# Kernel optimization log

Hardware: AMD Instinct MI355X
Metric: run time of the kernel (lower is better)

The kernel has to match this reference:

```python
import jax, jax.numpy as jnp
import numpy as np

D_MODEL = 1024
NHEAD = 16
DHEAD = D_MODEL // NHEAD
DFF = 4096
B, S = 2, 2048
R = 25                # local_attention_radius = 5*5
K = 5                 # rel_pos_max_distance
W = 2 * R + 1         # window width
EPS = 1e-5


def setup_inputs() -> dict:
    key = jax.random.key(0)
    ks = jax.random.split(key, 12)
    s = 0.02
    g = lambda k, shape: jax.random.normal(k, shape, jnp.float32) * s
    return {
        "src": jax.random.normal(ks[0], (B, S, D_MODEL), jnp.float32),
        # attention in/out projections (W stored [out,in], applied x @ W.T + b)
        "wq": g(ks[1], (D_MODEL, D_MODEL)), "bq": jnp.zeros((D_MODEL,), jnp.float32),
        "wk": g(ks[2], (D_MODEL, D_MODEL)), "bk": jnp.zeros((D_MODEL,), jnp.float32),
        "wv": g(ks[3], (D_MODEL, D_MODEL)), "bv": jnp.zeros((D_MODEL,), jnp.float32),
        "wo": g(ks[4], (D_MODEL, D_MODEL)), "bo": jnp.zeros((D_MODEL,), jnp.float32),
        # relative position embeddings, ids clipped to [-K, K] -> 2K+1 rows
        "rel_emb": g(ks[5], (2 * K + 1, DHEAD)),
        # FFN
        "w1": g(ks[6], (DFF, D_MODEL)), "b1": jnp.zeros((DFF,), jnp.float32),
        "w2": g(ks[7], (D_MODEL, DFF)), "b2": jnp.zeros((D_MODEL,), jnp.float32),
        # layernorms
        "g1": jnp.ones((D_MODEL,), jnp.float32), "beta1": jnp.zeros((D_MODEL,), jnp.float32),
        "g2": jnp.ones((D_MODEL,), jnp.float32), "beta2": jnp.zeros((D_MODEL,), jnp.float32),
    }


def _layernorm(x, g, b):
    m = x.mean(-1, keepdims=True)
    v = ((x - m) ** 2).mean(-1, keepdims=True)
    return (x - m) * jax.lax.rsqrt(v + EPS) * g + b


def _rel_window_attention(x, wq, bq, wk, bk, wv, bv, wo, bo, rel_emb):
    b, s, d = x.shape

    def proj(w, bias):
        return (x @ w.T + bias).reshape(b, s, NHEAD, DHEAD).transpose(0, 2, 1, 3)

    q = proj(wq, bq)  # [B,H,S,Dh]
    k = proj(wk, bk)
    v = proj(wv, bv)

    offsets = jnp.arange(-R, R + 1)                     # [W]
    j = jnp.arange(s)[:, None] + offsets[None, :]       # [S,W] absolute key index
    valid = (j >= 0) & (j < s)
    jc = jnp.clip(j, 0, s - 1)

    scale = 1.0 / np.sqrt(DHEAD).astype(np.float32)
    k_win = k[:, :, jc]                                 # [B,H,S,W,Dh] banded gather
    scores = jnp.einsum('bhsd,bhswd->bhsw', q, k_win) * scale
    rel_ids = jnp.clip(offsets, -K, K) + K              # [W]
    scores = scores + jnp.einsum('bhsd,wd->bhsw', q, rel_emb[rel_ids]) * scale
    scores = jnp.where(valid[None, None], scores, jnp.float32(-1e30))
    attn = jax.nn.softmax(scores, axis=-1)              # [B,H,S,W]

    v_win = v[:, :, jc]                                 # [B,H,S,W,Dh]
    out = jnp.einsum('bhsw,bhswd->bhsd', attn, v_win)
    out = out.transpose(0, 2, 1, 3).reshape(b, s, d)
    return out @ wo.T + bo


def reference(src, wq, bq, wk, bk, wv, bv, wo, bo, rel_emb,
              w1, b1, w2, b2, g1, beta1, g2, beta2):
    # post-norm (norm_first=False default) transformer block, dropout=0 (eval)
    z = _rel_window_attention(src, wq, bq, wk, bk, wv, bv, wo, bo, rel_emb)
    x = _layernorm(src + z, g1, beta1)
    ff = jax.nn.relu(x @ w1.T + b1) @ w2.T + b2
    return _layernorm(x + ff, g2, beta2)
```

## Files before the change

kernel.cpp:

```cpp
#include <hip/hip_runtime.h>


#define D_MODEL 1024
#define SEQ     2048
#define NROWS   4096
#define WIN     51
#define RAD     25

typedef __attribute__((ext_vector_type(8))) __bf16 bf16x8;
typedef __attribute__((ext_vector_type(4))) float  floatx4;

__device__ __forceinline__ unsigned short f2bf(float x) {
    unsigned u = __float_as_uint(x);
    unsigned r = u + 0x7fffu + ((u >> 16) & 1u);
    return (unsigned short)(r >> 16);
}
__device__ __forceinline__ float bf2f(unsigned short h) {
    return __uint_as_float(((unsigned)h) << 16);
}

__device__ __forceinline__ void gld16(const unsigned short* g, unsigned short* l) {
    __builtin_amdgcn_global_load_lds(
        (const __attribute__((address_space(1))) unsigned int*)g,
        (__attribute__((address_space(3))) unsigned int*)l,
        16, 0, 0);
}

__global__ __launch_bounds__(256) void cvt4(const float* __restrict__ in,
                                            unsigned short* __restrict__ out,
                                            int n4) {
    int i = blockIdx.x * 256 + threadIdx.x;
    if (i >= n4) return;
    float4 f = ((const float4*)in)[i];
    ushort4 u;
    u.x = f2bf(f.x); u.y = f2bf(f.y); u.z = f2bf(f.z); u.w = f2bf(f.w);
    ((ushort4*)out)[i] = u;
}

__global__ __launch_bounds__(256) void concat3(const float* __restrict__ a,
                                               const float* __restrict__ b,
                                               const float* __restrict__ c,
                                               float* __restrict__ out) {
    int i = blockIdx.x * 256 + threadIdx.x;
    if (i >= 3072) return;
    float v = (i < 1024) ? a[i] : (i < 2048 ? b[i - 1024] : c[i - 2048]);
    out[i] = v;
}

#define BM 128
#define BN 128
#define BK 64

__global__ __launch_bounds__(256, 2)
void gemm_bt(const unsigned short* __restrict__ A,
             const unsigned short* __restrict__ Wt,
             const float* __restrict__ bias,
             float* __restrict__ Cf,
             unsigned short* __restrict__ Cb,
             int K, int ldc, int relu)
{
    __shared__ __attribute__((aligned(16))) unsigned short As[2][BM * BK];
    __shared__ __attribute__((aligned(16))) unsigned short Bs[2][BN * BK];

    const int tid  = threadIdx.x;
    const int lane = tid & 63;
    const int wave = tid >> 6;
    const int bm = blockIdx.y * BM;
    const int bn = blockIdx.x * BN;
    const int wm = (wave >> 1) * 64;
    const int wn = (wave & 1) * 64;

    const int srow = lane >> 3;
    const int scol = ((lane & 7) ^ srow) * 8;
    const unsigned short* Ag = A  + (size_t)(bm + wave * 32 + srow) * K + scol;
    const unsigned short* Wg = Wt + (size_t)(bn + wave * 32 + srow) * K + scol;
    const size_t istep = (size_t)8 * K;
    const int lbase = wave * 2048;

    const int fm  = lane & 15;
    const int g4  = lane >> 4;
    const int fsw = fm & 7;

    floatx4 acc[4][4] = {};
    const int iters = K >> 6;

    #pragma unroll
    for (int t = 0; t < 4; t++) {
        gld16(Ag + t * istep, &As[0][lbase + t * 512]);
        gld16(Wg + t * istep, &Bs[0][lbase + t * 512]);
    }

    for (int i = 0; i < iters; i++) {
        const int cur = i & 1;
        __syncthreads();
        if (i + 1 < iters) {
            const int nxt = cur ^ 1;
            const unsigned short* Agn = Ag + (size_t)(i + 1) * BK;
            const unsigned short* Wgn = Wg + (size_t)(i + 1) * BK;
            #pragma unroll
            for (int t = 0; t < 4; t++) {
                gld16(Agn + t * istep, &As[nxt][lbase + t * 512]);
                gld16(Wgn + t * istep, &Bs[nxt][lbase + t * 512]);
            }
        }
        #pragma unroll
        for (int s = 0; s < 2; s++) {
            const int pg = ((s * 4 + g4) ^ fsw) * 8;
            bf16x8 af[4], bf[4];
            #pragma unroll
            for (int ii = 0; ii < 4; ii++)
                af[ii] = *(const bf16x8*)(&As[cur][(wm + ii * 16 + fm) * BK + pg]);
            #pragma unroll
            for (int j = 0; j < 4; j++)
                bf[j] = *(const bf16x8*)(&Bs[cur][(wn + j * 16 + fm) * BK + pg]);
            #pragma unroll
            for (int ii = 0; ii < 4; ii++)
                #pragma unroll
                for (int j = 0; j < 4; j++)
                    acc[ii][j] = __builtin_amdgcn_mfma_f32_16x16x32_bf16(
                        af[ii], bf[j], acc[ii][j], 0, 0, 0);
        }
    }

    const int r0 = bm + wm + (lane >> 4) * 4;
    const int c0e = bn + wn + (lane & 15);
    #pragma unroll
    for (int i = 0; i < 4; i++) {
        #pragma unroll
        for (int j = 0; j < 4; j++) {
            const int col = c0e + j * 16;
            const float bv = bias[col];
            #pragma unroll
            for (int r = 0; r < 4; r++) {
                const int row = r0 + i * 16 + r;
                float v = acc[i][j][r] + bv;
                if (relu) v = fmaxf(v, 0.0f);
                if (Cf) Cf[(size_t)row * ldc + col] = v;
                if (Cb) Cb[(size_t)row * ldc + col] = f2bf(v);
            }
        }
    }
}

__global__ __launch_bounds__(256, 2)
void attn_mfma(const unsigned short* __restrict__ qkv,
               const float* __restrict__ rel,
               unsigned short* __restrict__ attnb)
{
    __shared__ __attribute__((aligned(16))) unsigned short Qs[64 * 72];
    __shared__ __attribute__((aligned(16))) unsigned short Ks[128 * 72];
    __shared__ __attribute__((aligned(16))) unsigned short Vt[64 * 168];
    __shared__ __attribute__((aligned(16))) unsigned short Rs[16 * 72];
    __shared__ __attribute__((aligned(16))) unsigned short Pl[4 * 16 * 104];
    __shared__ float Qrl[4 * 16 * 12];

    const int t   = threadIdx.x;
    const int blk = blockIdx.x;
    const int st  = blk & 31;
    const int h   = (blk >> 5) & 15;
    const int b   = blk >> 9;
    const int s0  = st << 6;
    const int brow0 = b * SEQ;

    const int trow = t >> 3;
    const int tc   = (t & 7) * 8;
    const uint4 z4 = make_uint4(0, 0, 0, 0);

    #pragma unroll
    for (int p = 0; p < 2; p++) {
        int r = trow + p * 32;
        uint4 v = *(const uint4*)(qkv + (size_t)(brow0 + s0 + r) * 3072 + h * 64 + tc);
        *(uint4*)(Qs + r * 72 + tc) = v;
    }
    #pragma unroll
    for (int p = 0; p < 4; p++) {
        int kr = trow + p * 32;
        int ka = s0 - 25 + kr;
        bool in = (ka >= 0) & (ka < SEQ);
        uint4 kv = z4, vv = z4;
        if (in) {
            kv = *(const uint4*)(qkv + (size_t)(brow0 + ka) * 3072 + 1024 + h * 64 + tc);
            vv = *(const uint4*)(qkv + (size_t)(brow0 + ka) * 3072 + 2048 + h * 64 + tc);
        }
        *(uint4*)(Ks + kr * 72 + tc) = kv;
        const unsigned short* e = (const unsigned short*)&vv;
        #pragma unroll
        for (int j = 0; j < 8; j++)
            Vt[(tc + j) * 168 + kr] = e[j];
    }
    if (t < 176) {
        float4 f = ((const float4*)rel)[t];
        int fi = t * 4, rr = fi >> 6, cc = fi & 63;
        ushort4 u;
        u.x = f2bf(f.x); u.y = f2bf(f.y); u.z = f2bf(f.z); u.w = f2bf(f.w);
        *(ushort4*)(Rs + rr * 72 + cc) = u;
    } else {
        int fi = 704 + (t - 176) * 4, rr = fi >> 6, cc = fi & 63;
        *(ushort4*)(Rs + rr * 72 + cc) = make_ushort4(0, 0, 0, 0);
    }
    {
        int n = t * 4, w2 = n >> 8, rem = n & 255, rr = rem >> 4, cc = 80 + (rem & 15);
        *(ushort4*)(Pl + w2 * (16 * 104) + rr * 104 + cc) = make_ushort4(0, 0, 0, 0);
    }
    for (int idx = t; idx < 320; idx += 256) {
        int r = idx / 5, cchunk = idx % 5;
        *(uint4*)(Vt + r * 168 + 128 + cchunk * 8) = z4;
    }
    __syncthreads();

    const int wave = t >> 6;
    const int lane = t & 63;
    const int fm   = lane & 15;
    const int fk8  = (lane >> 4) * 8;
    const int S0w  = s0 + wave * 16;
    unsigned short* Plw = Pl + wave * (16 * 104);
    float* Ql = Qrl + wave * (16 * 12);

    bf16x8 qa0 = *(const bf16x8*)(Qs + (wave * 16 + fm) * 72 + fk8);
    bf16x8 qa1 = *(const bf16x8*)(Qs + (wave * 16 + fm) * 72 + fk8 + 32);

    floatx4 Sc[5];
    #pragma unroll
    for (int nt = 0; nt < 5; nt++) {
        bf16x8 kb0 = *(const bf16x8*)(Ks + (wave * 16 + nt * 16 + fm) * 72 + fk8);
        bf16x8 kb1 = *(const bf16x8*)(Ks + (wave * 16 + nt * 16 + fm) * 72 + fk8 + 32);
        floatx4 acc = {0.f, 0.f, 0.f, 0.f};
        acc = __builtin_amdgcn_mfma_f32_16x16x32_bf16(qa0, kb0, acc, 0, 0, 0);
        acc = __builtin_amdgcn_mfma_f32_16x16x32_bf16(qa1, kb1, acc, 0, 0, 0);
        Sc[nt] = acc;
    }
    {
        bf16x8 rb0 = *(const bf16x8*)(Rs + fm * 72 + fk8);
        bf16x8 rb1 = *(const bf16x8*)(Rs + fm * 72 + fk8 + 32);
        floatx4 qr = {0.f, 0.f, 0.f, 0.f};
        qr = __builtin_amdgcn_mfma_f32_16x16x32_bf16(qa0, rb0, qr, 0, 0, 0);
        qr = __builtin_amdgcn_mfma_f32_16x16x32_bf16(qa1, rb1, qr, 0, 0, 0);
        if (fm < 12) {
            #pragma unroll
            for (int reg = 0; reg < 4; reg++)
                Ql[((lane >> 4) * 4 + reg) * 12 + fm] = qr[reg];
        }
    }

    float inv[4];
    const int iq0 = (lane >> 4) * 4;
    #pragma unroll
    for (int reg = 0; reg < 4; reg++) {
        const int i = iq0 + reg;
        float sc[5];
        float mx = -1e30f;
        #pragma unroll
        for (int nt = 0; nt < 5; nt++) {
            int c   = nt * 16 + fm;
            int off = c - 25 - i;
            int ka  = S0w - 25 + c;
            bool valid = (off >= -RAD) & (off <= RAD) & (ka >= 0) & (ka < SEQ);
            int rid = min(max(off, -5), 5) + 5;
            float v = valid ? (Sc[nt][reg] + Ql[i * 12 + rid]) * 0.125f : -1e30f;
            sc[nt] = v;
            mx = fmaxf(mx, v);
        }
        #pragma unroll
        for (int o = 1; o < 16; o <<= 1) mx = fmaxf(mx, __shfl_xor(mx, o));
        float sum = 0.f;
        #pragma unroll
        for (int nt = 0; nt < 5; nt++) {
            float e = __expf(sc[nt] - mx);
            sum += e;
            Plw[i * 104 + nt * 16 + fm] = f2bf(e);
        }
        #pragma unroll
        for (int o = 1; o < 16; o <<= 1) sum += __shfl_xor(sum, o);
        inv[reg] = 1.0f / sum;
    }

    floatx4 O[4] = {};
    #pragma unroll
    for (int kc = 0; kc < 3; kc++) {
        bf16x8 pa = *(const bf16x8*)(Plw + fm * 104 + fk8 + kc * 32);
        #pragma unroll
        for (int nt = 0; nt < 4; nt++) {
            bf16x8 vb = *(const bf16x8*)(Vt + (nt * 16 + fm) * 168 + wave * 16 + fk8 + kc * 32);
            O[nt] = __builtin_amdgcn_mfma_f32_16x16x32_bf16(pa, vb, O[nt], 0, 0, 0);
        }
    }

    #pragma unroll
    for (int nt = 0; nt < 4; nt++) {
        const int d = nt * 16 + fm;
        #pragma unroll
        for (int reg = 0; reg < 4; reg++) {
            const int i = iq0 + reg;
            attnb[(size_t)(brow0 + S0w + i) * 1024 + h * 64 + d] = f2bf(O[nt][reg] * inv[reg]);
        }
    }
}

__global__ __launch_bounds__(256)
void ln_fuse(const float* __restrict__ af,
             const unsigned short* __restrict__ ab,
             const float* __restrict__ bres,
             const float* __restrict__ gamma,
             const float* __restrict__ beta,
             float* __restrict__ outf,
             unsigned short* __restrict__ outb)
{
    const int wave = threadIdx.x >> 6;
    const int lane = threadIdx.x & 63;
    const int row = blockIdx.x * 4 + wave;
    const size_t base = (size_t)row * D_MODEL;

    float x[16];
    float sum = 0.0f, sq = 0.0f;
    #pragma unroll
    for (int i = 0; i < 4; i++) {
        const int c4 = lane + i * 64;
        float4 vb = ((const float4*)(bres + base))[c4];
        float4 va;
        if (af) {
            va = ((const float4*)(af + base))[c4];
        } else {
            ushort4 ua = ((const ushort4*)(ab + base))[c4];
            va.x = bf2f(ua.x); va.y = bf2f(ua.y); va.z = bf2f(ua.z); va.w = bf2f(ua.w);
        }
        float e0 = va.x + vb.x, e1 = va.y + vb.y, e2 = va.z + vb.z, e3 = va.w + vb.w;
        x[i*4+0] = e0; x[i*4+1] = e1; x[i*4+2] = e2; x[i*4+3] = e3;
        sum += e0 + e1 + e2 + e3;
        sq  += e0*e0 + e1*e1 + e2*e2 + e3*e3;
    }
    #pragma unroll
    for (int off = 32; off > 0; off >>= 1) {
        sum += __shfl_xor(sum, off);
        sq  += __shfl_xor(sq,  off);
    }
    const float mean = sum * (1.0f / 1024.0f);
    const float var  = sq  * (1.0f / 1024.0f) - mean * mean;
    const float rs   = rsqrtf(var + 1e-5f);

    #pragma unroll
    for (int i = 0; i < 4; i++) {
        const int c4 = lane + i * 64;
        float4 g4 = ((const float4*)gamma)[c4];
        float4 b4 = ((const float4*)beta)[c4];
        float4 o;
        o.x = (x[i*4+0] - mean) * rs * g4.x + b4.x;
        o.y = (x[i*4+1] - mean) * rs * g4.y + b4.y;
        o.z = (x[i*4+2] - mean) * rs * g4.z + b4.z;
        o.w = (x[i*4+3] - mean) * rs * g4.w + b4.w;
        if (outf) ((float4*)(outf + base))[c4] = o;
        if (outb) {
            ushort4 u;
            u.x = f2bf(o.x); u.y = f2bf(o.y); u.z = f2bf(o.z); u.w = f2bf(o.w);
            ((ushort4*)(outb + base))[c4] = u;
        }
    }
}

extern "C" void kernel_launch(void* const* d_in, const int* in_sizes, int n_in,
                              void* d_out, int out_size, void* d_ws, size_t ws_size,
                              hipStream_t stream)
{
    const float* src = (const float*)d_in[0];
    const float* wq  = (const float*)d_in[1];
    const float* bq  = (const float*)d_in[2];
    const float* wk  = (const float*)d_in[3];
    const float* bk  = (const float*)d_in[4];
    const float* wv  = (const float*)d_in[5];
    const float* bv  = (const float*)d_in[6];
    const float* wo  = (const float*)d_in[7];
    const float* bo  = (const float*)d_in[8];
    const float* rel = (const float*)d_in[9];
    const float* w1  = (const float*)d_in[10];
    const float* b1  = (const float*)d_in[11];
    const float* w2  = (const float*)d_in[12];
    const float* b2  = (const float*)d_in[13];
    const float* g1  = (const float*)d_in[14];
    const float* be1 = (const float*)d_in[15];
    const float* g2  = (const float*)d_in[16];
    const float* be2 = (const float*)d_in[17];
    float* out = (float*)d_out;

    char* ws = (char*)d_ws;
    const size_t MB = 1048576;
    unsigned short* wqkvb = (unsigned short*)(ws + 0);
    unsigned short* wob   = (unsigned short*)(ws + 6  * MB);
    unsigned short* w1b   = (unsigned short*)(ws + 8  * MB);
    unsigned short* w2b   = (unsigned short*)(ws + 16 * MB);
    float*          bqkv  = (float*)         (ws + 24 * MB);
    unsigned short* xb    = (unsigned short*)(ws + 25 * MB);
    unsigned short* attnb = (unsigned short*)(ws + 25 * MB);
    unsigned short* qkvb  = (unsigned short*)(ws + 33 * MB);
    unsigned short* ff1b  = (unsigned short*)(ws + 33 * MB);
    float*          z     = (float*)         (ws + 65 * MB);
    float*          ff2   = (float*)         (ws + 65 * MB);
    unsigned short* x1b   = (unsigned short*)(ws + 81 * MB);

    cvt4<<<4096, 256, 0, stream>>>(src, xb, 1048576);
    cvt4<<<1024, 256, 0, stream>>>(wq, wqkvb,           262144);
    cvt4<<<1024, 256, 0, stream>>>(wk, wqkvb + 1048576, 262144);
    cvt4<<<1024, 256, 0, stream>>>(wv, wqkvb + 2097152, 262144);
    cvt4<<<1024, 256, 0, stream>>>(wo, wob, 262144);
    cvt4<<<4096, 256, 0, stream>>>(w1, w1b, 1048576);
    cvt4<<<4096, 256, 0, stream>>>(w2, w2b, 1048576);
    concat3<<<12, 256, 0, stream>>>(bq, bk, bv, bqkv);

    const dim3 blk(256);
    gemm_bt<<<dim3(3072 / BN, NROWS / BM), blk, 0, stream>>>(
        xb, wqkvb, bqkv, nullptr, qkvb, 1024, 3072, 0);
    attn_mfma<<<1024, blk, 0, stream>>>(qkvb, rel, attnb);
    gemm_bt<<<dim3(1024 / BN, NROWS / BM), blk, 0, stream>>>(
        attnb, wob, bo, z, nullptr, 1024, 1024, 0);
    ln_fuse<<<NROWS / 4, blk, 0, stream>>>(src, nullptr, z, g1, be1, nullptr, x1b);
    gemm_bt<<<dim3(4096 / BN, NROWS / BM), blk, 0, stream>>>(
        x1b, w1b, b1, nullptr, ff1b, 1024, 4096, 1);
    gemm_bt<<<dim3(1024 / BN, NROWS / BM), blk, 0, stream>>>(
        ff1b, w2b, b2, ff2, nullptr, 4096, 1024, 0);
    ln_fuse<<<NROWS / 4, blk, 0, stream>>>(nullptr, x1b, ff2, g2, be2, out, nullptr);
}
```

Measured before the change: 355.5 us.

## Split-K the N=1024 GEMMs, swizzle tile order, reduce partials in layernorm

The two narrow GEMMs (attention output projection and FFN down projection) now split K in two and write bf16 partial sums to separate slices. The layernorm kernel adds both partials and the bias, so the reduction is fused into an existing pass. All GEMMs switch to a 1D grid with a grouped tile mapping aimed at better L2 reuse, and the fp32 output path is dropped. The goal is to fill more CUs on the 256-tile GEMMs, at the cost of rounding partial sums to bf16 and more bytes written.

```diff
diff --git a/kernel.cpp b/kernel.cpp
--- a/kernel.cpp
+++ b/kernel.cpp
@@ -55,26 +55,33 @@
 void gemm_bt(const unsigned short* __restrict__ A,
              const unsigned short* __restrict__ Wt,
              const float* __restrict__ bias,
-             float* __restrict__ Cf,
              unsigned short* __restrict__ Cb,
-             int K, int ldc, int relu)
+             int kstride, int kloop, int T, int ldc, int relu)
 {
     __shared__ __attribute__((aligned(16))) unsigned short As[2][BM * BK];
     __shared__ __attribute__((aligned(16))) unsigned short Bs[2][BN * BK];
 
+    const int id = blockIdx.x;
+    const int s  = id / T;
+    const int t  = id - s * T;
+    const int sid  = (t & 7) * (T >> 3) + (t >> 3);
+    const int rect = sid >> 5;
+    const int r    = sid & 31;
+    const int bm = ((rect & 7) * 4 + (r >> 3)) * BM;
+    const int bn = ((rect >> 3) * 8 + (r & 7)) * BN;
+
     const int tid  = threadIdx.x;
     const int lane = tid & 63;
     const int wave = tid >> 6;
-    const int bm = blockIdx.y * BM;
-    const int bn = blockIdx.x * BN;
     const int wm = (wave >> 1) * 64;
     const int wn = (wave & 1) * 64;
 
     const int srow = lane >> 3;
     const int scol = ((lane & 7) ^ srow) * 8;
-    const unsigned short* Ag = A  + (size_t)(bm + wave * 32 + srow) * K + scol;
-    const unsigned short* Wg = Wt + (size_t)(bn + wave * 32 + srow) * K + scol;
-    const size_t istep = (size_t)8 * K;
+    const int kofs = s * kloop;
+    const unsigned short* Ag = A  + (size_t)(bm + wave * 32 + srow) * kstride + kofs + scol;
+    const unsigned short* Wg = Wt + (size_t)(bn + wave * 32 + srow) * kstride + kofs + scol;
+    const size_t istep = (size_t)8 * kstride;
     const int lbase = wave * 2048;
 
     const int fm  = lane & 15;
@@ -82,12 +89,12 @@
     const int fsw = fm & 7;
 
     floatx4 acc[4][4] = {};
-    const int iters = K >> 6;
-
-    #pragma unroll
-    for (int t = 0; t < 4; t++) {
-        gld16(Ag + t * istep, &As[0][lbase + t * 512]);
-        gld16(Wg + t * istep, &Bs[0][lbase + t * 512]);
+    const int iters = kloop >> 6;
+
+    #pragma unroll
+    for (int u = 0; u < 4; u++) {
+        gld16(Ag + u * istep, &As[0][lbase + u * 512]);
+        gld16(Wg + u * istep, &Bs[0][lbase + u * 512]);
     }
 
     for (int i = 0; i < iters; i++) {
@@ -98,14 +105,14 @@
             const unsigned short* Agn = Ag + (size_t)(i + 1) * BK;
             const unsigned short* Wgn = Wg + (size_t)(i + 1) * BK;
             #pragma unroll
-            for (int t = 0; t < 4; t++) {
-                gld16(Agn + t * istep, &As[nxt][lbase + t * 512]);
-                gld16(Wgn + t * istep, &Bs[nxt][lbase + t * 512]);
+            for (int u = 0; u < 4; u++) {
+                gld16(Agn + u * istep, &As[nxt][lbase + u * 512]);
+                gld16(Wgn + u * istep, &Bs[nxt][lbase + u * 512]);
             }
         }
         #pragma unroll
-        for (int s = 0; s < 2; s++) {
-            const int pg = ((s * 4 + g4) ^ fsw) * 8;
+        for (int sh = 0; sh < 2; sh++) {
+            const int pg = ((sh * 4 + g4) ^ fsw) * 8;
             bf16x8 af[4], bf[4];
             #pragma unroll
             for (int ii = 0; ii < 4; ii++)
@@ -122,6 +129,7 @@
         }
     }
 
+    unsigned short* Co = Cb + (size_t)s * NROWS * ldc;
     const int r0 = bm + wm + (lane >> 4) * 4;
     const int c0e = bn + wn + (lane & 15);
     #pragma unroll
@@ -129,14 +137,13 @@
         #pragma unroll
         for (int j = 0; j < 4; j++) {
             const int col = c0e + j * 16;
-            const float bv = bias[col];
-            #pragma unroll
-            for (int r = 0; r < 4; r++) {
-                const int row = r0 + i * 16 + r;
-                float v = acc[i][j][r] + bv;
+            const float bv = bias ? bias[col] : 0.0f;
+            #pragma unroll
+            for (int rr = 0; rr < 4; rr++) {
+                const int row = r0 + i * 16 + rr;
+                float v = acc[i][j][rr] + bv;
                 if (relu) v = fmaxf(v, 0.0f);
-                if (Cf) Cf[(size_t)row * ldc + col] = v;
-                if (Cb) Cb[(size_t)row * ldc + col] = f2bf(v);
+                Co[(size_t)row * ldc + col] = f2bf(v);
             }
         }
     }
@@ -297,9 +304,11 @@
 }
 
 __global__ __launch_bounds__(256)
-void ln_fuse(const float* __restrict__ af,
-             const unsigned short* __restrict__ ab,
-             const float* __restrict__ bres,
+void ln_fuse(const float* __restrict__ resf,
+             const unsigned short* __restrict__ resb,
+             const unsigned short* __restrict__ p0,
+             const unsigned short* __restrict__ p1,
+             const float* __restrict__ cbias,
              const float* __restrict__ gamma,
              const float* __restrict__ beta,
              float* __restrict__ outf,
@@ -315,15 +324,20 @@
     #pragma unroll
     for (int i = 0; i < 4; i++) {
         const int c4 = lane + i * 64;
-        float4 vb = ((const float4*)(bres + base))[c4];
+        ushort4 u0 = ((const ushort4*)(p0 + base))[c4];
+        ushort4 u1 = ((const ushort4*)(p1 + base))[c4];
+        float4 cb = ((const float4*)cbias)[c4];
         float4 va;
-        if (af) {
-            va = ((const float4*)(af + base))[c4];
+        if (resf) {
+            va = ((const float4*)(resf + base))[c4];
         } else {
-            ushort4 ua = ((const ushort4*)(ab + base))[c4];
+            ushort4 ua = ((const ushort4*)(resb + base))[c4];
             va.x = bf2f(ua.x); va.y = bf2f(ua.y); va.z = bf2f(ua.z); va.w = bf2f(ua.w);
         }
-        float e0 = va.x + vb.x, e1 = va.y + vb.y, e2 = va.z + vb.z, e3 = va.w + vb.w;
+        float e0 = va.x + bf2f(u0.x) + bf2f(u1.x) + cb.x;
+        float e1 = va.y + bf2f(u0.y) + bf2f(u1.y) + cb.y;
+        float e2 = va.z + bf2f(u0.z) + bf2f(u1.z) + cb.z;
+        float e3 = va.w + bf2f(u0.w) + bf2f(u1.w) + cb.w;
         x[i*4+0] = e0; x[i*4+1] = e1; x[i*4+2] = e2; x[i*4+3] = e3;
         sum += e0 + e1 + e2 + e3;
         sq  += e0*e0 + e1*e1 + e2*e2 + e3*e3;
@@ -390,10 +404,11 @@
     unsigned short* xb    = (unsigned short*)(ws + 25 * MB);
     unsigned short* attnb = (unsigned short*)(ws + 25 * MB);
     unsigned short* qkvb  = (unsigned short*)(ws + 33 * MB);
+    unsigned short* z01   = (unsigned short*)(ws + 33 * MB);
     unsigned short* ff1b  = (unsigned short*)(ws + 33 * MB);
-    float*          z     = (float*)         (ws + 65 * MB);
-    float*          ff2   = (float*)         (ws + 65 * MB);
+    unsigned short* f01   = (unsigned short*)(ws + 65 * MB);
     unsigned short* x1b   = (unsigned short*)(ws + 81 * MB);
+    const size_t SL = (size_t)NROWS * 1024;
 
     cvt4<<<4096, 256, 0, stream>>>(src, xb, 1048576);
     cvt4<<<1024, 256, 0, stream>>>(wq, wqkvb,           262144);
@@ -405,15 +420,13 @@
     concat3<<<12, 256, 0, stream>>>(bq, bk, bv, bqkv);
 
     const dim3 blk(256);
-    gemm_bt<<<dim3(3072 / BN, NROWS / BM), blk, 0, stream>>>(
-        xb, wqkvb, bqkv, nullptr, qkvb, 1024, 3072, 0);
+    gemm_bt<<<768, blk, 0, stream>>>(xb, wqkvb, bqkv, qkvb, 1024, 1024, 768, 3072, 0);
     attn_mfma<<<1024, blk, 0, stream>>>(qkvb, rel, attnb);
-    gemm_bt<<<dim3(1024 / BN, NROWS / BM), blk, 0, stream>>>(
-        attnb, wob, bo, z, nullptr, 1024, 1024, 0);
-    ln_fuse<<<NROWS / 4, blk, 0, stream>>>(src, nullptr, z, g1, be1, nullptr, x1b);
-    gemm_bt<<<dim3(4096 / BN, NROWS / BM), blk, 0, stream>>>(
-        x1b, w1b, b1, nullptr, ff1b, 1024, 4096, 1);
-    gemm_bt<<<dim3(1024 / BN, NROWS / BM), blk, 0, stream>>>(
-        ff1b, w2b, b2, ff2, nullptr, 4096, 1024, 0);
-    ln_fuse<<<NROWS / 4, blk, 0, stream>>>(nullptr, x1b, ff2, g2, be2, out, nullptr);
-}
+    gemm_bt<<<512, blk, 0, stream>>>(attnb, wob, nullptr, z01, 1024, 512, 256, 1024, 0);
+    ln_fuse<<<NROWS / 4, blk, 0, stream>>>(src, nullptr, z01, z01 + SL, bo, g1, be1,
+                                           nullptr, x1b);
+    gemm_bt<<<1024, blk, 0, stream>>>(x1b, w1b, b1, ff1b, 1024, 1024, 1024, 4096, 1);
+    gemm_bt<<<512, blk, 0, stream>>>(ff1b, w2b, nullptr, f01, 4096, 2048, 256, 1024, 0);
+    ln_fuse<<<NROWS / 4, blk, 0, stream>>>(nullptr, x1b, f01, f01 + SL, b2, g2, be2,
+                                           out, nullptr);
+}
```

Result: faster. 322.0 us (-9.4%).
